# Kernel tuning notes

Hardware: AMD Instinct MI355X
Metric: run time of the kernel (lower is better)

Reference implementation:

```python
import jax, jax.numpy as jnp
import numpy as np
from jax import lax

DN = ('NCHW', 'OIHW', 'NCHW')
SAME = ((1, 1), (1, 1))
VALID = ((0, 0), (0, 0))


def conv(x, w, pad):
    return lax.conv_general_dilated(x, w, (1, 1), pad, dimension_numbers=DN)


def convT(x, w, strides):
    # inverse (transposed) conv; for kernel==stride this exactly inverts the
    # non-overlapping pooling rulebook used by spconv's SparseInverseConv2d
    return lax.conv_transpose(x, w, strides, 'VALID', dimension_numbers=DN)


def maxpool(x, k):
    return lax.reduce_window(x, -jnp.inf, lax.max, (1, 1) + k, (1, 1) + k, 'VALID')


def lrelu(x):
    return jnp.where(x >= 0, x, 0.01 * x)  # F.leaky_relu default slope


def setup_inputs() -> dict:
    key = jax.random.key(0)
    ks = jax.random.split(key, 14)
    B, C, H, W = 32, 6, 500, 128
    x = jax.random.normal(ks[0], (B, C, H, W), jnp.float32)  # fully dense => all voxels active

    def p(k, shape):
        return jax.random.normal(k, shape, jnp.float32) * 0.05

    return {
        'x': x,
        'w1': p(ks[1], (8, 6, 3, 3)),      # SubMConv2d 6->8
        'w2': p(ks[2], (16, 8, 3, 3)),     # SubMConv2d 8->16
        'w3': p(ks[3], (32, 16, 3, 3)),    # SubMConv2d 16->32
        'wmu': p(ks[4], (1, 32, 1, 5)),    # SparseConv2d 32->1, kernel (1,5)
        'wlv': p(ks[5], (1, 32, 1, 5)),
        'wu0': p(ks[6], (32, 1, 1, 5)),    # SparseInverseConv2d 1->32
        'wu1': p(ks[7], (32, 32, 5, 2)),   # inverse of pool3
        'w4': p(ks[8], (16, 32, 3, 3)),
        'wu2': p(ks[9], (16, 16, 5, 2)),   # inverse of pool2
        'w5': p(ks[10], (8, 16, 3, 3)),
        'wu3': p(ks[11], (8, 8, 2, 2)),    # inverse of pool1
        'w6': p(ks[12], (6, 8, 3, 3)),
    }


def reference(x, w1, w2, w3, wmu, wlv, wu0, wu1, w4, wu2, w5, wu3, w6):
    B = x.shape[0]
    # ---- encoder ----
    h = lrelu(conv(x, w1, SAME))        # [B,8,500,128]
    h = maxpool(h, (2, 2))              # [B,8,250,64]
    h = lrelu(conv(h, w2, SAME))        # [B,16,250,64]
    h = maxpool(h, (5, 2))              # [B,16,50,32]
    h = lrelu(conv(h, w3, SAME))        # [B,32,50,32]
    h = maxpool(h, (5, 2))              # [B,32,10,16]
    mu = conv(h, wmu, VALID)            # [B,1,10,12]
    logvar = conv(h, wlv, VALID)        # [B,1,10,12]
    # ---- reparameterise ----
    eps = jax.random.normal(jax.random.key(42), mu.shape, mu.dtype)
    z = mu + eps * jnp.exp(0.5 * logvar)
    # ---- decoder ----
    d = lrelu(convT(z, wu0, (1, 1)))    # [B,32,10,16]
    d = lrelu(convT(d, wu1, (5, 2)))    # [B,32,50,32]
    d = lrelu(conv(d, w4, SAME))        # [B,16,50,32]
    d = lrelu(convT(d, wu2, (5, 2)))    # [B,16,250,64]
    d = lrelu(conv(d, w5, SAME))        # [B,8,250,64]
    d = lrelu(convT(d, wu3, (2, 2)))    # [B,8,500,128]
    d = lrelu(conv(d, w6, SAME))        # [B,6,500,128]
    return (d, mu.reshape(B, -1), logvar.reshape(B, -1), z.reshape(B, -1))
```

## Files before the change

kernel.cpp:

```cpp
#include <hip/hip_runtime.h>
#include <stdint.h>

#define DI __device__ __forceinline__

DI float lrelu(float x){ return x >= 0.0f ? x : 0.01f*x; }

DI uint32_t rotl32(uint32_t x, int d){ return (x << d) | (x >> (32 - d)); }

DI void threefry_0_42(uint32_t& x0, uint32_t& x1){
  const uint32_t ks0 = 0u, ks1 = 42u, ks2 = 0x1BD11BF0u;
  x0 += ks0; x1 += ks1;
  #define TFR(d) { x0 += x1; x1 = rotl32(x1,(d)); x1 ^= x0; }
  TFR(13) TFR(15) TFR(26) TFR(6)  x0 += ks1; x1 += ks2 + 1u;
  TFR(17) TFR(29) TFR(16) TFR(24) x0 += ks2; x1 += ks0 + 2u;
  TFR(13) TFR(15) TFR(26) TFR(6)  x0 += ks0; x1 += ks1 + 3u;
  TFR(17) TFR(29) TFR(16) TFR(24) x0 += ks1; x1 += ks2 + 4u;
  TFR(13) TFR(15) TFR(26) TFR(6)  x0 += ks2; x1 += ks0 + 5u;
  #undef TFR
}

DI float erfinv_f32(float x){
  float w = -log1pf(-x*x);
  float p;
  if (w < 5.0f){
    w = w - 2.5f;
    p = 2.81022636e-08f;
    p = fmaf(p, w, 3.43273939e-07f);
    p = fmaf(p, w, -3.5233877e-06f);
    p = fmaf(p, w, -4.39150654e-06f);
    p = fmaf(p, w, 0.00021858087f);
    p = fmaf(p, w, -0.00125372503f);
    p = fmaf(p, w, -0.00417768164f);
    p = fmaf(p, w, 0.246640727f);
    p = fmaf(p, w, 1.50140941f);
  } else {
    w = sqrtf(w) - 3.0f;
    p = -0.000200214257f;
    p = fmaf(p, w, 0.000100950558f);
    p = fmaf(p, w, 0.00134934322f);
    p = fmaf(p, w, -0.00367342844f);
    p = fmaf(p, w, 0.00573950773f);
    p = fmaf(p, w, -0.0076224613f);
    p = fmaf(p, w, 0.00943887047f);
    p = fmaf(p, w, 1.00167406f);
    p = fmaf(p, w, 2.83297682f);
  }
  return p * x;
}

#define OUT_D_OFF   0
#define OUT_MU_OFF  12288000
#define OUT_LV_OFF  (12288000 + 3840)
#define OUT_Z_OFF   (12288000 + 7680)

__global__ __launch_bounds__(256) void k_enc1(const float* __restrict__ x,
                                              const float* __restrict__ w1,
                                              float* __restrict__ p1){
  __shared__ float tile[6*10*130];
  int tid = threadIdx.x;
  int band = blockIdx.x % 63;
  int b    = blockIdx.x / 63;
  int r0 = band*8;
  for (int idx = tid; idx < 6*10*130; idx += 256){
    int lc = idx % 130;
    int rest = idx / 130;
    int lr = rest % 10;
    int ch = rest / 10;
    int gr = r0 - 1 + lr, gc = lc - 1;
    float v = 0.0f;
    if ((unsigned)gr < 500u && (unsigned)gc < 128u)
      v = x[((b*6+ch)*500+gr)*128+gc];
    tile[idx] = v;
  }
  __syncthreads();
  int pw = tid & 63, pr = tid >> 6;
  int ph = band*4 + pr;
  float acc[2][2][8];
  #pragma unroll
  for (int a=0;a<2;a++)
    #pragma unroll
    for (int d=0;d<2;d++)
      #pragma unroll
      for (int o=0;o<8;o++) acc[a][d][o] = 0.0f;
  int base = (2*pr)*130 + 2*pw;
  #pragma unroll 2
  for (int c = 0; c < 6; ++c){
    float win[4][4];
    #pragma unroll
    for (int i=0;i<4;i++)
      #pragma unroll
      for (int j=0;j<4;j++)
        win[i][j] = tile[c*1300 + base + i*130 + j];
    #pragma unroll
    for (int kh=0;kh<3;kh++)
      #pragma unroll
      for (int kw=0;kw<3;kw++){
        float wv[8];
        #pragma unroll
        for (int o=0;o<8;o++) wv[o] = w1[((o*6+c)*3+kh)*3+kw];
        #pragma unroll
        for (int dy=0;dy<2;dy++)
          #pragma unroll
          for (int dx=0;dx<2;dx++){
            float v = win[dy+kh][dx+kw];
            #pragma unroll
            for (int o=0;o<8;o++) acc[dy][dx][o] = fmaf(v, wv[o], acc[dy][dx][o]);
          }
      }
  }
  if (ph < 250){
    #pragma unroll
    for (int o=0;o<8;o++){
      float m = fmaxf(fmaxf(acc[0][0][o], acc[0][1][o]), fmaxf(acc[1][0][o], acc[1][1][o]));
      p1[((b*8+o)*250+ph)*64+pw] = lrelu(m);
    }
  }
}

__global__ __launch_bounds__(256) void k_enc2(const float* __restrict__ in,
                                              const float* __restrict__ w2,
                                              float* __restrict__ p2){
  __shared__ float tile[8*22*66];
  int tid = threadIdx.x;
  int band = blockIdx.x % 13;
  int b    = blockIdx.x / 13;
  int r0 = band*20;
  for (int idx = tid; idx < 8*22*66; idx += 256){
    int lc = idx % 66;
    int rest = idx / 66;
    int lr = rest % 22;
    int ch = rest / 22;
    int gr = r0 - 1 + lr, gc = lc - 1;
    float v = 0.0f;
    if ((unsigned)gr < 250u && (unsigned)gc < 64u)
      v = in[((b*8+ch)*250+gr)*64+gc];
    tile[idx] = v;
  }
  __syncthreads();
  int dx = tid & 1; int u = tid >> 1;
  int pw = u & 31; int pr = (u >> 5) & 3;
  int cw = 2*pw + dx;
  int ph = band*4 + pr;
  float acc[5][16];
  #pragma unroll
  for (int dy=0;dy<5;dy++)
    #pragma unroll
    for (int o=0;o<16;o++) acc[dy][o] = 0.0f;
  int base = (5*pr)*66 + cw;
  #pragma unroll 1
  for (int c = 0; c < 8; ++c){
    float win[7][3];
    #pragma unroll
    for (int i=0;i<7;i++)
      #pragma unroll
      for (int j=0;j<3;j++)
        win[i][j] = tile[c*1452 + base + i*66 + j];
    #pragma unroll
    for (int kh=0;kh<3;kh++)
      #pragma unroll
      for (int kw=0;kw<3;kw++){
        float wv[16];
        #pragma unroll
        for (int o=0;o<16;o++) wv[o] = w2[((o*8+c)*3+kh)*3+kw];
        #pragma unroll
        for (int dy=0;dy<5;dy++){
          float v = win[dy+kh][kw];
          #pragma unroll
          for (int o=0;o<16;o++) acc[dy][o] = fmaf(v, wv[o], acc[dy][o]);
        }
      }
  }
  #pragma unroll
  for (int o=0;o<16;o++){
    float m = acc[0][o];
    #pragma unroll
    for (int dy=1;dy<5;dy++) m = fmaxf(m, acc[dy][o]);
    m = fmaxf(m, __shfl_xor(m, 1));
    if (dx == 0 && ph < 50) p2[((b*16+o)*50+ph)*32+pw] = lrelu(m);
  }
}

__global__ __launch_bounds__(256) void k_conv3(const float* __restrict__ in,
                                               const float* __restrict__ w3,
                                               float* __restrict__ outp){
  __shared__ float tile[16*10*34];
  int tid = threadIdx.x;
  int bi = blockIdx.x;
  int band = bi % 7; int oh = (bi/7) & 1; int b = bi / 14;
  int r0 = band*8;
  for (int idx = tid; idx < 16*10*34; idx += 256){
    int lc = idx % 34;
    int rest = idx / 34;
    int lr = rest % 10;
    int ch = rest / 10;
    int gr = r0 - 1 + lr, gc = lc - 1;
    float v = 0.0f;
    if ((unsigned)gr < 50u && (unsigned)gc < 32u)
      v = in[((b*16+ch)*50+gr)*32+gc];
    tile[idx] = v;
  }
  __syncthreads();
  int col = tid & 31, tr = tid >> 5;
  int h = r0 + tr;
  float acc[16];
  #pragma unroll
  for (int o=0;o<16;o++) acc[o] = 0.0f;
  int base = tr*34 + col;
  #pragma unroll 2
  for (int c = 0; c < 16; ++c){
    float win[3][3];
    #pragma unroll
    for (int i=0;i<3;i++)
      #pragma unroll
      for (int j=0;j<3;j++)
        win[i][j] = tile[c*340 + base + i*34 + j];
    #pragma unroll
    for (int kh=0;kh<3;kh++)
      #pragma unroll
      for (int kw=0;kw<3;kw++){
        float v = win[kh][kw];
        #pragma unroll
        for (int o=0;o<16;o++)
          acc[o] = fmaf(v, w3[(((oh*16+o)*16+c)*3+kh)*3+kw], acc[o]);
      }
  }
  if (h < 50){
    #pragma unroll
    for (int o=0;o<16;o++)
      outp[((b*32 + oh*16 + o)*50 + h)*32 + col] = lrelu(acc[o]);
  }
}

__global__ __launch_bounds__(256) void k_pool3(const float* __restrict__ in,
                                               float* __restrict__ outp){
  int t = blockIdx.x*256 + threadIdx.x;
  int pw = t & 15; int u = t >> 4; int ph = u % 10; u /= 10; int o = u & 31; int b = u >> 5;
  float m = -INFINITY;
  #pragma unroll
  for (int dh=0;dh<5;dh++)
    #pragma unroll
    for (int dw=0;dw<2;dw++)
      m = fmaxf(m, in[((b*32+o)*50 + 5*ph+dh)*32 + 2*pw+dw]);
  outp[((b*32+o)*10+ph)*16+pw] = m;
}

__global__ __launch_bounds__(256) void k_latent(const float* __restrict__ p3,
                                                const float* __restrict__ wmu,
                                                const float* __restrict__ wlv,
                                                float* __restrict__ outp){
  int t = blockIdx.x*256 + threadIdx.x;
  int w = t % 12; int h = (t/12) % 10; int b = t/120;
  float mu = 0.0f, lv = 0.0f;
  for (int c = 0; c < 32; ++c){
    const float* row = p3 + ((b*32+c)*10+h)*16 + w;
    #pragma unroll
    for (int kw=0;kw<5;kw++){
      float v = row[kw];
      mu = fmaf(v, wmu[c*5+kw], mu);
      lv = fmaf(v, wlv[c*5+kw], lv);
    }
  }
  uint32_t x0 = 0u, x1 = (uint32_t)t;
  threefry_0_42(x0, x1);
  uint32_t bits = x0 ^ x1;
  float f = __uint_as_float((bits >> 9) | 0x3f800000u) - 1.0f;
  const float lo = -0.99999994f;
  float uu = fmaxf(lo, f * 2.0f + lo);
  float eps = 1.41421356f * erfinv_f32(uu);
  float z = mu + eps * expf(0.5f * lv);
  outp[OUT_MU_OFF + t] = mu;
  outp[OUT_LV_OFF + t] = lv;
  outp[OUT_Z_OFF  + t] = z;
}

__global__ __launch_bounds__(256) void k_dec0(const float* __restrict__ outp,
                                              const float* __restrict__ wu0,
                                              float* __restrict__ d0){
  int t = blockIdx.x*256 + threadIdx.x;
  int w = t & 15; int u = t >> 4; int h = u % 10; u /= 10; int o = u & 31; int b = u >> 5;
  const float* z = outp + OUT_Z_OFF;
  float a = 0.0f;
  #pragma unroll
  for (int kw=0;kw<5;kw++){
    int ww = w + kw - 4;
    if ((unsigned)ww < 12u) a = fmaf(z[b*120 + h*12 + ww], wu0[o*5+kw], a);
  }
  d0[((b*32+o)*10+h)*16+w] = lrelu(a);
}

__global__ __launch_bounds__(256) void k_dec1(const float* __restrict__ d0,
                                              const float* __restrict__ wu1,
                                              float* __restrict__ d1){
  int t = blockIdx.x*256 + threadIdx.x;
  int wo = t & 31; int u = t >> 5; int ho = u % 50; u /= 50; int og = u & 3; int b = u >> 2;
  int i = ho / 5, r = ho - 5*i, jj = wo >> 1, s = wo & 1;
  const float* ip = d0 + b*5120 + i*16 + jj;
  float in[32];
  #pragma unroll
  for (int c=0;c<32;c++) in[c] = ip[c*160];
  #pragma unroll
  for (int oo=0;oo<8;oo++){
    int o = og*8 + oo;
    const float* wp = wu1 + (o*32*5 + (4-r))*2 + (1-s);
    float a = 0.0f;
    #pragma unroll
    for (int c=0;c<32;c++) a = fmaf(in[c], wp[c*10], a);
    d1[((b*32+o)*50+ho)*32+wo] = lrelu(a);
  }
}

__global__ __launch_bounds__(256) void k_c4(const float* __restrict__ in,
                                            const float* __restrict__ w4,
                                            float* __restrict__ outp){
  __shared__ float tile[32*10*34];
  int tid = threadIdx.x;
  int bi = blockIdx.x;
  int band = bi % 7; int oh = (bi/7) & 1; int b = bi / 14;
  int r0 = band*8;
  for (int idx = tid; idx < 32*10*34; idx += 256){
    int lc = idx % 34;
    int rest = idx / 34;
    int lr = rest % 10;
    int ch = rest / 10;
    int gr = r0 - 1 + lr, gc = lc - 1;
    float v = 0.0f;
    if ((unsigned)gr < 50u && (unsigned)gc < 32u)
      v = in[((b*32+ch)*50+gr)*32+gc];
    tile[idx] = v;
  }
  __syncthreads();
  int col = tid & 31, tr = tid >> 5;
  int h = r0 + tr;
  float acc[8];
  #pragma unroll
  for (int o=0;o<8;o++) acc[o] = 0.0f;
  int base = tr*34 + col;
  #pragma unroll 2
  for (int c = 0; c < 32; ++c){
    float win[3][3];
    #pragma unroll
    for (int i=0;i<3;i++)
      #pragma unroll
      for (int j=0;j<3;j++)
        win[i][j] = tile[c*340 + base + i*34 + j];
    #pragma unroll
    for (int kh=0;kh<3;kh++)
      #pragma unroll
      for (int kw=0;kw<3;kw++){
        float v = win[kh][kw];
        #pragma unroll
        for (int o=0;o<8;o++)
          acc[o] = fmaf(v, w4[(((oh*8+o)*32+c)*3+kh)*3+kw], acc[o]);
      }
  }
  if (h < 50){
    #pragma unroll
    for (int o=0;o<8;o++)
      outp[((b*16 + oh*8 + o)*50 + h)*32 + col] = lrelu(acc[o]);
  }
}

__global__ __launch_bounds__(256) void k_u2(const float* __restrict__ d2,
                                            const float* __restrict__ wu2,
                                            float* __restrict__ d3){
  int t = blockIdx.x*256 + threadIdx.x;
  int w = t & 63; int u = t >> 6; int h = u % 250; int b = u / 250;
  int i = h / 5, r = h - 5*i, jj = w >> 1, s = w & 1;
  const float* ip = d2 + b*25600 + i*32 + jj;
  float in[16];
  #pragma unroll
  for (int c=0;c<16;c++) in[c] = ip[c*1600];
  #pragma unroll
  for (int o=0;o<16;o++){
    const float* wp = wu2 + (o*16*5 + (4-r))*2 + (1-s);
    float a = 0.0f;
    #pragma unroll
    for (int c=0;c<16;c++) a = fmaf(in[c], wp[c*10], a);
    d3[((b*16+o)*250+h)*64+w] = lrelu(a);
  }
}

__global__ __launch_bounds__(256) void k_c5(const float* __restrict__ in,
                                            const float* __restrict__ w5,
                                            float* __restrict__ outp){
  __shared__ float tile[16*10*66];
  int tid = threadIdx.x;
  int band = blockIdx.x % 32;
  int b    = blockIdx.x / 32;
  int r0 = band*8;
  for (int idx = tid; idx < 16*10*66; idx += 256){
    int lc = idx % 66;
    int rest = idx / 66;
    int lr = rest % 10;
    int ch = rest / 10;
    int gr = r0 - 1 + lr, gc = lc - 1;
    float v = 0.0f;
    if ((unsigned)gr < 250u && (unsigned)gc < 64u)
      v = in[((b*16+ch)*250+gr)*64+gc];
    tile[idx] = v;
  }
  __syncthreads();
  int cp = tid & 31, tr = tid >> 5;
  int h = r0 + tr;
  float acc[2][8];
  #pragma unroll
  for (int dx=0;dx<2;dx++)
    #pragma unroll
    for (int o=0;o<8;o++) acc[dx][o] = 0.0f;
  int base = tr*66 + 2*cp;
  #pragma unroll 2
  for (int c = 0; c < 16; ++c){
    float win[3][4];
    #pragma unroll
    for (int i=0;i<3;i++)
      #pragma unroll
      for (int j=0;j<4;j++)
        win[i][j] = tile[c*660 + base + i*66 + j];
    #pragma unroll
    for (int kh=0;kh<3;kh++)
      #pragma unroll
      for (int kw=0;kw<3;kw++){
        float wv[8];
        #pragma unroll
        for (int o=0;o<8;o++) wv[o] = w5[((o*16+c)*3+kh)*3+kw];
        #pragma unroll
        for (int dx=0;dx<2;dx++){
          float v = win[kh][dx+kw];
          #pragma unroll
          for (int o=0;o<8;o++) acc[dx][o] = fmaf(v, wv[o], acc[dx][o]);
        }
      }
  }
  if (h < 250){
    #pragma unroll
    for (int dx=0;dx<2;dx++)
      #pragma unroll
      for (int o=0;o<8;o++)
        outp[((b*8+o)*250+h)*64 + 2*cp+dx] = lrelu(acc[dx][o]);
  }
}

__global__ __launch_bounds__(256) void k_u3(const float* __restrict__ d4,
                                            const float* __restrict__ wu3,
                                            float* __restrict__ d5){
  int t = blockIdx.x*256 + threadIdx.x;
  int w = t & 127; int u = t >> 7; int h = u % 500; int b = u / 500;
  int i = h >> 1, r = h & 1, jj = w >> 1, s = w & 1;
  const float* ip = d4 + b*128000 + i*64 + jj;
  float in[8];
  #pragma unroll
  for (int c=0;c<8;c++) in[c] = ip[c*16000];
  #pragma unroll
  for (int o=0;o<8;o++){
    const float* wp = wu3 + (o*8*2 + (1-r))*2 + (1-s);
    float a = 0.0f;
    #pragma unroll
    for (int c=0;c<8;c++) a = fmaf(in[c], wp[c*4], a);
    d5[((b*8+o)*500+h)*128+w] = lrelu(a);
  }
}

__global__ __launch_bounds__(256) void k_c6(const float* __restrict__ in,
                                            const float* __restrict__ w6,
                                            float* __restrict__ outp){
  __shared__ float tile[8*10*130];
  int tid = threadIdx.x;
  int band = blockIdx.x % 63;
  int b    = blockIdx.x / 63;
  int r0 = band*8;
  for (int idx = tid; idx < 8*10*130; idx += 256){
    int lc = idx % 130;
    int rest = idx / 130;
    int lr = rest % 10;
    int ch = rest / 10;
    int gr = r0 - 1 + lr, gc = lc - 1;
    float v = 0.0f;
    if ((unsigned)gr < 500u && (unsigned)gc < 128u)
      v = in[((b*8+ch)*500+gr)*128+gc];
    tile[idx] = v;
  }
  __syncthreads();
  int cp = tid & 63, rp = tid >> 6;
  float acc[2][2][6];
  #pragma unroll
  for (int dy=0;dy<2;dy++)
    #pragma unroll
    for (int dx=0;dx<2;dx++)
      #pragma unroll
      for (int o=0;o<6;o++) acc[dy][dx][o] = 0.0f;
  int base = (2*rp)*130 + 2*cp;
  #pragma unroll 2
  for (int c = 0; c < 8; ++c){
    float win[4][4];
    #pragma unroll
    for (int i=0;i<4;i++)
      #pragma unroll
      for (int j=0;j<4;j++)
        win[i][j] = tile[c*1300 + base + i*130 + j];
    #pragma unroll
    for (int kh=0;kh<3;kh++)
      #pragma unroll
      for (int kw=0;kw<3;kw++){
        float wv[6];
        #pragma unroll
        for (int o=0;o<6;o++) wv[o] = w6[((o*8+c)*3+kh)*3+kw];
        #pragma unroll
        for (int dy=0;dy<2;dy++)
          #pragma unroll
          for (int dx=0;dx<2;dx++){
            float v = win[dy+kh][dx+kw];
            #pragma unroll
            for (int o=0;o<6;o++) acc[dy][dx][o] = fmaf(v, wv[o], acc[dy][dx][o]);
          }
      }
  }
  #pragma unroll
  for (int dy=0;dy<2;dy++){
    int h = r0 + 2*rp + dy;
    if (h < 500){
      #pragma unroll
      for (int dx=0;dx<2;dx++)
        #pragma unroll
        for (int o=0;o<6;o++)
          outp[((b*6+o)*500+h)*128 + 2*cp+dx] = lrelu(acc[dy][dx][o]);
    }
  }
}

extern "C" void kernel_launch(void* const* d_in, const int* in_sizes, int n_in,
                              void* d_out, int out_size, void* d_ws, size_t ws_size,
                              hipStream_t stream){
  const float* x   = (const float*)d_in[0];
  const float* w1  = (const float*)d_in[1];
  const float* w2  = (const float*)d_in[2];
  const float* w3  = (const float*)d_in[3];
  const float* wmu = (const float*)d_in[4];
  const float* wlv = (const float*)d_in[5];
  const float* wu0 = (const float*)d_in[6];
  const float* wu1 = (const float*)d_in[7];
  const float* w4  = (const float*)d_in[8];
  const float* wu2 = (const float*)d_in[9];
  const float* w5  = (const float*)d_in[10];
  const float* wu3 = (const float*)d_in[11];
  const float* w6  = (const float*)d_in[12];
  float* out = (float*)d_out;
  float* A  = (float*)d_ws;
  float* Bb = A + 4096000;

  k_enc1 <<<2016, 256, 0, stream>>>(x,  w1,  A);
  k_enc2 <<< 416, 256, 0, stream>>>(A,  w2,  Bb);
  k_conv3<<< 448, 256, 0, stream>>>(Bb, w3,  A);
  k_pool3<<< 640, 256, 0, stream>>>(A,  Bb);
  k_latent<<< 15, 256, 0, stream>>>(Bb, wmu, wlv, out);
  k_dec0 <<< 640, 256, 0, stream>>>(out, wu0, A);
  k_dec1 <<< 800, 256, 0, stream>>>(A,  wu1, Bb);
  k_c4   <<< 448, 256, 0, stream>>>(Bb, w4,  A);
  k_u2   <<<2000, 256, 0, stream>>>(A,  wu2, Bb);
  k_c5   <<<1024, 256, 0, stream>>>(Bb, w5,  A);
  k_u3   <<<8000, 256, 0, stream>>>(A,  wu3, Bb);
  k_c6   <<<2016, 256, 0, stream>>>(Bb, w6,  out);
}
```

Baseline: 432.2 us.

## Fuse final transposed conv into last 3x3 conv via shared-memory tile

The 2x2 transposed convolution producing the 8x500x128 decoder activation is now computed directly into shared memory inside the final 3x3 conv kernel, so the full-resolution intermediate is never written to or read back from global memory. The conv thread mapping also changes to one row by four columns per thread, using float4 shared loads and float4 global stores. Halo rows are recomputed by neighbouring blocks, and the wu3 weights are staged in shared memory.

```diff
diff --git a/kernel.cpp b/kernel.cpp
--- a/kernel.cpp
+++ b/kernel.cpp
@@ -440,89 +440,91 @@
   }
 }
 
-__global__ __launch_bounds__(256) void k_u3(const float* __restrict__ d4,
-                                            const float* __restrict__ wu3,
-                                            float* __restrict__ d5){
-  int t = blockIdx.x*256 + threadIdx.x;
-  int w = t & 127; int u = t >> 7; int h = u % 500; int b = u / 500;
-  int i = h >> 1, r = h & 1, jj = w >> 1, s = w & 1;
-  const float* ip = d4 + b*128000 + i*64 + jj;
-  float in[8];
-  #pragma unroll
-  for (int c=0;c<8;c++) in[c] = ip[c*16000];
-  #pragma unroll
-  for (int o=0;o<8;o++){
-    const float* wp = wu3 + (o*8*2 + (1-r))*2 + (1-s);
-    float a = 0.0f;
-    #pragma unroll
-    for (int c=0;c<8;c++) a = fmaf(in[c], wp[c*4], a);
-    d5[((b*8+o)*500+h)*128+w] = lrelu(a);
-  }
-}
-
-__global__ __launch_bounds__(256) void k_c6(const float* __restrict__ in,
-                                            const float* __restrict__ w6,
-                                            float* __restrict__ outp){
-  __shared__ float tile[8*10*130];
+__global__ __launch_bounds__(256) void k_u3c6(const float* __restrict__ d4,
+                                              const float* __restrict__ wu3,
+                                              const float* __restrict__ w6,
+                                              float* __restrict__ outp){
+  __shared__ __align__(16) float dt[8*10*132];
+  __shared__ __align__(16) float wl[256];
   int tid = threadIdx.x;
   int band = blockIdx.x % 63;
   int b    = blockIdx.x / 63;
   int r0 = band*8;
-  for (int idx = tid; idx < 8*10*130; idx += 256){
-    int lc = idx % 130;
-    int rest = idx / 130;
-    int lr = rest % 10;
-    int ch = rest / 10;
-    int gr = r0 - 1 + lr, gc = lc - 1;
-    float v = 0.0f;
-    if ((unsigned)gr < 500u && (unsigned)gc < 128u)
-      v = in[((b*8+ch)*500+gr)*128+gc];
-    tile[idx] = v;
-  }
-  __syncthreads();
-  int cp = tid & 63, rp = tid >> 6;
-  float acc[2][2][6];
-  #pragma unroll
-  for (int dy=0;dy<2;dy++)
-    #pragma unroll
-    for (int dx=0;dx<2;dx++)
-      #pragma unroll
-      for (int o=0;o<6;o++) acc[dy][dx][o] = 0.0f;
-  int base = (2*rp)*130 + 2*cp;
+  wl[tid] = wu3[tid];
+  if (tid < 80){
+    int ch = tid / 10, lr = tid % 10;
+    dt[(ch*10+lr)*132 + 128] = 0.0f;
+    dt[(ch*10+lr)*132 + 129] = 0.0f;
+  }
+  __syncthreads();
+  for (int s = tid; s < 320; s += 256){
+    int q = s & 31, lr = s >> 5;
+    int h = r0 - 1 + lr;
+    if ((unsigned)h < 500u){
+      int i2 = h >> 1, r = h & 1;
+      float2 dv[8];
+      #pragma unroll
+      for (int c=0;c<8;c++)
+        dv[c] = *(const float2*)(d4 + ((b*8+c)*250 + i2)*64 + 2*q);
+      int wbase = (1-r)*2;
+      #pragma unroll
+      for (int o5=0;o5<8;o5++){
+        float a0=0.f,a1=0.f,a2=0.f,a3=0.f;
+        #pragma unroll
+        for (int c=0;c<8;c++){
+          float2 wp = *(const float2*)(wl + o5*32 + c*4 + wbase);
+          a0 = fmaf(dv[c].x, wp.y, a0);
+          a1 = fmaf(dv[c].x, wp.x, a1);
+          a2 = fmaf(dv[c].y, wp.y, a2);
+          a3 = fmaf(dv[c].y, wp.x, a3);
+        }
+        float4 v4 = make_float4(lrelu(a0), lrelu(a1), lrelu(a2), lrelu(a3));
+        *(float4*)(dt + (o5*10+lr)*132 + 4*q) = v4;
+      }
+    } else {
+      float4 z = make_float4(0.f,0.f,0.f,0.f);
+      #pragma unroll
+      for (int o5=0;o5<8;o5++)
+        *(float4*)(dt + (o5*10+lr)*132 + 4*q) = z;
+    }
+  }
+  __syncthreads();
+  int q = tid & 31, tr = tid >> 5;
+  int R = r0 + tr;
+  float acc[4][6];
+  #pragma unroll
+  for (int j=0;j<4;j++)
+    #pragma unroll
+    for (int o=0;o<6;o++) acc[j][o] = 0.0f;
+  int left = (q==0) ? 129 : (4*q - 1);
   #pragma unroll 2
-  for (int c = 0; c < 8; ++c){
-    float win[4][4];
-    #pragma unroll
-    for (int i=0;i<4;i++)
-      #pragma unroll
-      for (int j=0;j<4;j++)
-        win[i][j] = tile[c*1300 + base + i*130 + j];
-    #pragma unroll
-    for (int kh=0;kh<3;kh++)
+  for (int ch=0; ch<8; ++ch){
+    #pragma unroll
+    for (int wr=0; wr<3; ++wr){
+      const float* row = dt + (ch*10 + tr + wr)*132;
+      float win[6];
+      float4 m = *(const float4*)(row + 4*q);
+      win[0] = row[left];
+      win[1] = m.x; win[2] = m.y; win[3] = m.z; win[4] = m.w;
+      win[5] = row[4*q + 4];
       #pragma unroll
       for (int kw=0;kw<3;kw++){
-        float wv[6];
-        #pragma unroll
-        for (int o=0;o<6;o++) wv[o] = w6[((o*8+c)*3+kh)*3+kw];
-        #pragma unroll
-        for (int dy=0;dy<2;dy++)
+        #pragma unroll
+        for (int o=0;o<6;o++){
+          float wv = w6[((o*8+ch)*3+wr)*3+kw];
           #pragma unroll
-          for (int dx=0;dx<2;dx++){
-            float v = win[dy+kh][dx+kw];
-            #pragma unroll
-            for (int o=0;o<6;o++) acc[dy][dx][o] = fmaf(v, wv[o], acc[dy][dx][o]);
-          }
-      }
-  }
-  #pragma unroll
-  for (int dy=0;dy<2;dy++){
-    int h = r0 + 2*rp + dy;
-    if (h < 500){
-      #pragma unroll
-      for (int dx=0;dx<2;dx++)
-        #pragma unroll
-        for (int o=0;o<6;o++)
-          outp[((b*6+o)*500+h)*128 + 2*cp+dx] = lrelu(acc[dy][dx][o]);
+          for (int j=0;j<4;j++)
+            acc[j][o] = fmaf(win[j+kw], wv, acc[j][o]);
+        }
+      }
+    }
+  }
+  if (R < 500){
+    #pragma unroll
+    for (int o=0;o<6;o++){
+      float4 v = make_float4(lrelu(acc[0][o]), lrelu(acc[1][o]),
+                             lrelu(acc[2][o]), lrelu(acc[3][o]));
+      *(float4*)(outp + ((b*6+o)*500 + R)*128 + 4*q) = v;
     }
   }
 }
@@ -557,6 +559,5 @@
   k_c4   <<< 448, 256, 0, stream>>>(Bb, w4,  A);
   k_u2   <<<2000, 256, 0, stream>>>(A,  wu2, Bb);
   k_c5   <<<1024, 256, 0, stream>>>(Bb, w5,  A);
-  k_u3   <<<8000, 256, 0, stream>>>(A,  wu3, Bb);
-  k_c6   <<<2016, 256, 0, stream>>>(Bb, w6,  out);
-}
+  k_u3c6 <<<2016, 256, 0, stream>>>(A, wu3, w6, out);
+}
```

Result: faster. 381.0 us (-11.9%).
